# Optimization experiments

Hardware: AMD Instinct MI355X
Metric: run time of the kernel (lower is better)

Reference implementation:

```python
import jax, jax.numpy as jnp
import numpy as np

NUM_EMB = 100000   # v2e embedding table rows
EMB_DIM = 128      # embed_dim
N_EDGES = 320000   # total flattened neighbors (sum of len(to_neighs[i]))
N_NODES = 10000    # len(nodes)


def setup_inputs() -> dict:
    key = jax.random.key(0)
    k1, k2, k3 = jax.random.split(key, 3)
    weight = jax.random.normal(k1, (NUM_EMB, EMB_DIM), dtype=jnp.float32)
    neigh_idx = jax.random.randint(k2, (N_EDGES,), 0, NUM_EMB, dtype=jnp.int32)
    segment_ids = jnp.sort(jax.random.randint(k3, (N_EDGES,), 0, N_NODES, dtype=jnp.int32))
    return {"weight": weight, "neigh_idx": neigh_idx,
            "segment_ids": segment_ids, "num_nodes": N_NODES}


def reference(weight, neigh_idx, segment_ids, num_nodes):
    # Ragged gather: e_v = v2e.weight[to_neighs[i]] for all nodes, flattened. [E, D]
    gathered = weight[neigh_idx]
    # Segment-mean replaces the per-node torch.mean(e_v, dim=0) loop.
    sums = jax.ops.segment_sum(gathered, segment_ids, num_segments=num_nodes)  # [N, D]
    counts = jax.ops.segment_sum(jnp.ones((segment_ids.shape[0],), dtype=weight.dtype),
                                 segment_ids, num_segments=num_nodes)          # [N]
    to_feats = sums / jnp.maximum(counts, 1.0)[:, None]
    return to_feats
```

## Files before the change

kernel.cpp:

```cpp
#include <hip/hip_runtime.h>
#include <hip/hip_bf16.h>

#define EMB_DIM 128

__global__ void seg_starts_kernel(const int* __restrict__ seg, int E, int N,
                                  int* __restrict__ start) {
    int n = blockIdx.x * blockDim.x + threadIdx.x;
    if (n > N) return;
    int lo = 0, hi = E;
    while (lo < hi) {
        int mid = (lo + hi) >> 1;
        if (seg[mid] < n) lo = mid + 1; else hi = mid;
    }
    start[n] = lo;
}

__global__ void seg_mean_kernel(const float* __restrict__ W,
                                const int* __restrict__ idx,
                                const int* __restrict__ start,
                                float* __restrict__ out) {
    int n = blockIdx.x;
    int d = threadIdx.x;
    int s = start[n];
    int e = start[n + 1];
    float acc = 0.0f;
    int j = s;
    for (; j + 1 < e; j += 2) {
        int r0 = idx[j];
        int r1 = idx[j + 1];
        float a0 = W[(long long)r0 * EMB_DIM + d];
        float a1 = W[(long long)r1 * EMB_DIM + d];
        acc += a0;
        acc += a1;
    }
    if (j < e) {
        int r0 = idx[j];
        acc += W[(long long)r0 * EMB_DIM + d];
    }
    float cnt = (float)(e - s);
    out[n * EMB_DIM + d] = acc / fmaxf(cnt, 1.0f);
}

extern "C" void kernel_launch(void* const* d_in, const int* in_sizes, int n_in,
                              void* d_out, int out_size, void* d_ws, size_t ws_size,
                              hipStream_t stream) {
    const float* weight      = (const float*)d_in[0];
    const int*   neigh_idx   = (const int*)d_in[1];
    const int*   segment_ids = (const int*)d_in[2];
    int N = out_size / EMB_DIM;
    int E = in_sizes[1];

    int* start = (int*)d_ws;

    {
        int threads = 256;
        int blocks = (N + 1 + threads - 1) / threads;
        seg_starts_kernel<<<blocks, threads, 0, stream>>>(segment_ids, E, N, start);
    }
    {
        seg_mean_kernel<<<N, EMB_DIM, 0, stream>>>(weight, neigh_idx, start, (float*)d_out);
    }
}
```

Measured before the change: 112.5 us.

## Split segment rows across 8 thread groups with float4 loads and shared reduction

The segment-mean kernel now uses 256 threads per node, split into 8 groups of 32 lanes. Each lane loads a float4 slice of an embedding row, and each group takes every eighth neighbor of the segment. Partial sums are then combined through shared memory and written as float4. This exposes more concurrent row gathers per node to hide memory latency and widens each load, at the cost of a syncthreads, a shared-memory reduction, and idle groups on short segments.

New measurement: 112.3 us. About the same (-0.3%).

```diff
diff --git a/kernel.cpp b/kernel.cpp
--- a/kernel.cpp
+++ b/kernel.cpp
@@ -20,25 +20,35 @@
                                 const int* __restrict__ start,
                                 float* __restrict__ out) {
     int n = blockIdx.x;
-    int d = threadIdx.x;
+    int t = threadIdx.x;
+    int g = t >> 5;
+    int c = t & 31;
     int s = start[n];
     int e = start[n + 1];
-    float acc = 0.0f;
-    int j = s;
-    for (; j + 1 < e; j += 2) {
-        int r0 = idx[j];
-        int r1 = idx[j + 1];
-        float a0 = W[(long long)r0 * EMB_DIM + d];
-        float a1 = W[(long long)r1 * EMB_DIM + d];
-        acc += a0;
-        acc += a1;
+
+    float4 acc = make_float4(0.f, 0.f, 0.f, 0.f);
+    for (int j = s + g; j < e; j += 8) {
+        int r = idx[j];
+        const float4* row = (const float4*)(W + (long long)r * EMB_DIM);
+        float4 v = row[c];
+        acc.x += v.x; acc.y += v.y; acc.z += v.z; acc.w += v.w;
     }
-    if (j < e) {
-        int r0 = idx[j];
-        acc += W[(long long)r0 * EMB_DIM + d];
+
+    __shared__ float4 red[8][32];
+    red[g][c] = acc;
+    __syncthreads();
+
+    if (g == 0) {
+        float4 a = red[0][c];
+        #pragma unroll
+        for (int gg = 1; gg < 8; ++gg) {
+            float4 v = red[gg][c];
+            a.x += v.x; a.y += v.y; a.z += v.z; a.w += v.w;
+        }
+        float inv = 1.0f / fmaxf((float)(e - s), 1.0f);
+        float4 o = make_float4(a.x * inv, a.y * inv, a.z * inv, a.w * inv);
+        ((float4*)(out + (long long)n * EMB_DIM))[c] = o;
     }
-    float cnt = (float)(e - s);
-    out[n * EMB_DIM + d] = acc / fmaxf(cnt, 1.0f);
 }
 
 extern "C" void kernel_launch(void* const* d_in, const int* in_sizes, int n_in,
@@ -58,6 +68,6 @@
         seg_starts_kernel<<<blocks, threads, 0, stream>>>(segment_ids, E, N, start);
     }
     {
-        seg_mean_kernel<<<N, EMB_DIM, 0, stream>>>(weight, neigh_idx, start, (float*)d_out);
+        seg_mean_kernel<<<N, 256, 0, stream>>>(weight, neigh_idx, start, (float*)d_out);
     }
 }
```
